# Optimization experiments

Hardware: AMD Instinct MI355X
Metric: run time of the kernel (lower is better)

The kernel has to match this reference:

```python
import jax, jax.numpy as jnp
import numpy as np

B, N = 16, 2048
EMB_DIM = 512
K = 20          # neighbor_num
S = 1           # support_num

def _norm(x, axis):
    # F.normalize: x / max(||x||, 1e-12)
    return x / jnp.maximum(jnp.linalg.norm(x, axis=axis, keepdims=True), 1e-12)

def knn(verts, k):
    # verts: (b, v, 3); squared-distance knn excluding self
    inner = jnp.einsum('bvd,bwd->bvw', verts, verts)
    quad = jnp.sum(verts * verts, axis=2)
    dist = quad[:, :, None] - 2.0 * inner + quad[:, None, :]
    _, idx = jax.lax.top_k(-dist, k + 1)
    return idx[:, :, 1:]

def gather_nb(x, idx):
    # x: (b, v, c), idx: (b, v, n) -> (b, v, n, c)
    return jax.vmap(lambda t, i: t[i])(x, idx)

def dir_norm(verts, idx):
    d = gather_nb(verts, idx) - verts[:, :, None, :]
    return _norm(d, -1)

def conv_surface(idx, verts, directions, kernel_num):
    theta = jax.nn.relu(jnp.einsum('bvnd,dk->bvnk', dir_norm(verts, idx), _norm(directions, 0)))
    b, v, n, _ = theta.shape
    theta = theta.reshape(b, v, n, S, kernel_num)
    return jnp.sum(jnp.max(theta, axis=2), axis=2)  # (b, v, kernel_num)

def conv_layer(idx, verts, fm, w, bias, directions, out_ch):
    theta = jax.nn.relu(jnp.einsum('bvnd,dk->bvnk', dir_norm(verts, idx), _norm(directions, 0)))
    feat = fm @ w + bias                            # (b, v, (S+1)*out_ch)
    center = feat[:, :, :out_ch]
    support = gather_nb(feat[:, :, out_ch:], idx)   # (b, v, n, S*out_ch)
    b, v, n, _ = support.shape
    act = (theta * support).reshape(b, v, n, S, out_ch)
    return center + jnp.sum(jnp.max(act, axis=2), axis=2)

def pool_layer(verts, fm, key, pooling_rate=4, neighbor_num=4):
    b, v, _ = verts.shape
    idx = knn(verts, neighbor_num)
    pooled = jnp.max(gather_nb(fm, idx), axis=2)
    samp = jax.random.permutation(key, v)[: v // pooling_rate]
    return verts[:, samp, :], pooled[:, samp, :]

def _forward(xyz, w1, b1, w2, b2, w3, b3, w4, b4, fcw, fcb, dir0,
             wc1, bc1, dir1, wc2, bc2, dir2, wc3, bc3, dir3, wc4, bc4, dir4,
             clw1, clb1, bn_gamma, bn_beta, clw2, clb2):
    relu = jax.nn.relu
    # PointNet trunk (Conv1d with kernel 1 == per-point matmul)
    x = relu(jnp.einsum('oc,bcn->bon', w1, xyz) + b1[None, :, None])
    x = relu(jnp.einsum('oc,bcn->bon', w2, x) + b2[None, :, None])
    gf = jnp.max(x, axis=2, keepdims=True)
    x = jnp.concatenate([x, jnp.broadcast_to(gf, x.shape)], axis=1)
    x = relu(jnp.einsum('oc,bcn->bon', w3, x) + b3[None, :, None])
    x = relu(jnp.einsum('oc,bcn->bon', w4, x) + b4[None, :, None])
    x = jnp.max(x, axis=2)                          # (B, 1024)
    # GCN3D trunk
    verts = jnp.transpose(xyz, (0, 2, 1))           # (B, N, 3)
    idx = knn(verts, K)
    fm0 = relu(conv_surface(idx, verts, dir0, 32))
    fm1 = relu(conv_layer(idx, verts, fm0, wc1, bc1, dir1, 64))
    verts, fm1 = pool_layer(verts, fm1, jax.random.key(1))
    idx = knn(verts, K)
    fm2 = relu(conv_layer(idx, verts, fm1, wc2, bc2, dir2, 128))
    fm3 = relu(conv_layer(idx, verts, fm2, wc3, bc3, dir3, 256))
    verts, fm3 = pool_layer(verts, fm3, jax.random.key(2))
    idx = knn(verts, K)
    fm4 = conv_layer(idx, verts, fm3, wc4, bc4, dir4, 1024)
    fg = jnp.max(fm4, axis=1)                       # (B, 1024)
    fc_data = jnp.concatenate([x, fg], axis=1)      # (B, 2048)
    embedding = fc_data @ fcw.T + fcb
    # classifier, eval mode: Dropout -> identity; BN uses running mean 0 / var 1
    h = fc_data @ clw1.T + clb1
    h = relu(h / jnp.sqrt(1.0 + 1e-5) * bn_gamma + bn_beta)
    pred = h @ clw2.T + clb2
    return embedding, pred

def setup_inputs():
    key = jax.random.key(0)
    ks = jax.random.split(key, 32)
    rn = lambda k, shp: jax.random.normal(k, shp, dtype=jnp.float32) * 0.05
    return {
        'xyz': jax.random.normal(ks[0], (B, 3, N), dtype=jnp.float32),
        'w1': rn(ks[1], (64, 3)), 'b1': rn(ks[2], (64,)),
        'w2': rn(ks[3], (128, 64)), 'b2': rn(ks[4], (128,)),
        'w3': rn(ks[5], (256, 256)), 'b3': rn(ks[6], (256,)),
        'w4': rn(ks[7], (1024, 256)), 'b4': rn(ks[8], (1024,)),
        'fcw': rn(ks[9], (EMB_DIM, 2048)), 'fcb': rn(ks[10], (EMB_DIM,)),
        'dir0': rn(ks[11], (3, 32)),
        'wc1': rn(ks[12], (32, 128)), 'bc1': rn(ks[13], (128,)), 'dir1': rn(ks[14], (3, 64)),
        'wc2': rn(ks[15], (64, 256)), 'bc2': rn(ks[16], (256,)), 'dir2': rn(ks[17], (3, 128)),
        'wc3': rn(ks[18], (128, 512)), 'bc3': rn(ks[19], (512,)), 'dir3': rn(ks[20], (3, 256)),
        'wc4': rn(ks[21], (256, 2048)), 'bc4': rn(ks[22], (2048,)), 'dir4': rn(ks[23], (3, 1024)),
        'clw1': rn(ks[24], (512, 2048)), 'clb1': rn(ks[25], (512,)),
        'bn_gamma': jnp.ones((512,), dtype=jnp.float32),
        'bn_beta': jnp.zeros((512,), dtype=jnp.float32),
        'clw2': rn(ks[26], (6, 512)), 'clb2': rn(ks[27], (6,)),
    }

def reference(xyz, w1, b1, w2, b2, w3, b3, w4, b4, fcw, fcb, dir0, wc1, bc1, dir1, wc2, bc2, dir2, wc3, bc3, dir3, wc4, bc4, dir4, clw1, clb1, bn_gamma, bn_beta, clw2, clb2):
    return _forward(xyz, w1, b1, w2, b2, w3, b3, w4, b4, fcw, fcb, dir0, wc1, bc1, dir1, wc2, bc2, dir2, wc3, bc3, dir3, wc4, bc4, dir4, clw1, clb1, bn_gamma, bn_beta, clw2, clb2)
```

## Files before the change

kernel.cpp:

```cpp
#include <hip/hip_runtime.h>
#include <hip/hip_bf16.h>
#include <math.h>

#define BB 16
#define NN 2048

typedef __attribute__((ext_vector_type(8))) short s8v;
typedef __attribute__((ext_vector_type(4))) float f4v;

__global__ void k_sentinel(float* o, int n, float v){
  int i = blockIdx.x*256 + threadIdx.x;
  if (i < n) o[i] = v;
}

__device__ __forceinline__ ushort f2bf(float x){
  unsigned u = __float_as_uint(x);
  unsigned r = u + 0x7FFFu + ((u>>16)&1u);
  return (ushort)(r>>16);
}
__device__ __forceinline__ void splitbf(float v, ushort &h, ushort &l){
  h = f2bf(v);
  float hf = __uint_as_float((unsigned)h<<16);
  l = f2bf(v-hf);
}


__global__ void k_wsrm(const float* __restrict__ src, ushort* __restrict__ dh,
                       ushort* __restrict__ dl, int total){
  int id = blockIdx.x*256 + threadIdx.x;
  if (id >= total) return;
  ushort h,l; splitbf(src[id], h, l);
  dh[id]=h; dl[id]=l;
}

__global__ void k_wstr(const float* __restrict__ src, ushort* __restrict__ dh,
                       ushort* __restrict__ dl, int K, int C){
  int id = blockIdx.x*256 + threadIdx.x;
  if (id >= K*C) return;
  int c = id % C, k = id / C;
  ushort h,l; splitbf(src[id], h, l);
  dh[(size_t)c*K + k]=h; dl[(size_t)c*K + k]=l;
}


__global__ void k_mlp1s(const float* __restrict__ xyz, const float* __restrict__ w1,
                        const float* __restrict__ b1, ushort* __restrict__ xh,
                        ushort* __restrict__ xl){
  int id = blockIdx.x*256 + threadIdx.x;
  if (id >= BB*NN*64) return;
  int o = id & 63, n = (id>>6) & (NN-1), b = id>>17;
  float acc = b1[o];
  #pragma unroll
  for (int c=0;c<3;c++)
    acc += w1[o*3+c] * xyz[(size_t)(b*3+c)*NN + n];
  acc = fmaxf(acc, 0.f);
  ushort h,l; splitbf(acc, h, l);
  xh[id]=h; xl[id]=l;
}

__global__ __launch_bounds__(256) void k_rowmax(const float* __restrict__ x, float* __restrict__ o,
                                                ushort* __restrict__ gh, ushort* __restrict__ gl, int cols){
  __shared__ float sm[256];
  int row = blockIdx.x, t = threadIdx.x;
  const float* xr = x + (size_t)row*cols;
  float m = -INFINITY;
  for (int c=t;c<cols;c+=256) m = fmaxf(m, xr[c]);
  sm[t]=m; __syncthreads();
  for (int s=128;s>0;s>>=1){ if (t<s) sm[t]=fmaxf(sm[t], sm[t+s]); __syncthreads(); }
  if (!t){
    o[row]=sm[0];
    ushort h,l; splitbf(sm[0], h, l);
    gh[row]=h; gl[row]=l;
  }
}

template<int EPI, int RELU, int BCOL>
__global__ __launch_bounds__(256) void k_bgemm(
    const ushort* __restrict__ Ahg, const ushort* __restrict__ Alg,
    const ushort* __restrict__ Bhg, const ushort* __restrict__ Blg,
    const ushort* __restrict__ gfh, const ushort* __restrict__ gfl,
    const float* __restrict__ bias,
    float* __restrict__ outp, float* __restrict__ pmaxp,
    ushort* __restrict__ oth, ushort* __restrict__ otl,
    int K, int ksplit, int Kb, int N, size_t sBT, size_t sOut, int M)
{
  __shared__ ushort Ah[128][40], Al[128][40];
  __shared__ ushort Bh[64][40],  Bl[64][40];
  __shared__ float red[2][128];
  int t = threadIdx.x, z = blockIdx.z;
  int o0 = blockIdx.y*128, n0 = blockIdx.x*64;
  int wid = t>>6, lane = t&63;
  int wm = wid>>1, wn = wid&1;
  int lr = lane&15, kg = lane>>4;

  f4v acc[4][2];
  #pragma unroll
  for (int i=0;i<4;i++)
    #pragma unroll
    for (int j=0;j<2;j++) acc[i][j] = (f4v){0.f,0.f,0.f,0.f};

  for (int k0=0; k0<K; k0+=32){
    __syncthreads();
    #pragma unroll
    for (int i=0;i<2;i++){
      int j = i*256+t, oo = j>>2, k8 = (j&3)*8;
      size_t sp = (size_t)(o0+oo)*K + k0 + k8;
      *(s8v*)&Ah[oo][k8] = *(const s8v*)(Ahg+sp);
      *(s8v*)&Al[oo][k8] = *(const s8v*)(Alg+sp);
    }
    {
      int nn = t>>2, k8 = (t&3)*8, gk = k0+k8;
      const ushort *sh, *sl;
      if (gk < ksplit){
        size_t sp = (size_t)z*sBT + (size_t)(n0+nn)*Kb + gk;
        sh = Bhg+sp; sl = Blg+sp;
      } else {
        size_t sp = (size_t)z*(K-ksplit) + (gk-ksplit);
        sh = gfh+sp; sl = gfl+sp;
      }
      *(s8v*)&Bh[nn][k8] = *(const s8v*)sh;
      *(s8v*)&Bl[nn][k8] = *(const s8v*)sl;
    }
    __syncthreads();

    s8v ah[4], al[4], bh[2], bl[2];
    #pragma unroll
    for (int mt=0;mt<4;mt++){
      int row = wm*64 + mt*16 + lr;
      ah[mt] = *(const s8v*)&Ah[row][kg*8];
      al[mt] = *(const s8v*)&Al[row][kg*8];
    }
    #pragma unroll
    for (int nt=0;nt<2;nt++){
      int col = wn*32 + nt*16 + lr;
      bh[nt] = *(const s8v*)&Bh[col][kg*8];
      bl[nt] = *(const s8v*)&Bl[col][kg*8];
    }
    #pragma unroll
    for (int mt=0;mt<4;mt++)
      #pragma unroll
      for (int nt=0;nt<2;nt++){
        acc[mt][nt] = __builtin_amdgcn_mfma_f32_16x16x32_bf16(ah[mt], bh[nt], acc[mt][nt], 0,0,0);
        acc[mt][nt] = __builtin_amdgcn_mfma_f32_16x16x32_bf16(ah[mt], bl[nt], acc[mt][nt], 0,0,0);
        acc[mt][nt] = __builtin_amdgcn_mfma_f32_16x16x32_bf16(al[mt], bh[nt], acc[mt][nt], 0,0,0);
      }
  }

  if (EPI == 1){
    #pragma unroll
    for (int mt=0;mt<4;mt++){
      #pragma unroll
      for (int e=0;e<4;e++){
        int row = o0 + wm*64 + mt*16 + kg*4 + e;
        float bv = bias[row];
        float m = fmaxf(fmaxf(acc[mt][0][e]+bv, 0.f), fmaxf(acc[mt][1][e]+bv, 0.f));
        m = fmaxf(m, __shfl_xor(m, 1, 64));
        m = fmaxf(m, __shfl_xor(m, 2, 64));
        m = fmaxf(m, __shfl_xor(m, 4, 64));
        m = fmaxf(m, __shfl_xor(m, 8, 64));
        if (lr == 0) red[wn][wm*64 + mt*16 + kg*4 + e] = m;
      }
    }
    __syncthreads();
    if (t < 128){
      float m = fmaxf(red[0][t], red[1][t]);
      pmaxp[((size_t)z*M + o0 + t)*gridDim.x + blockIdx.x] = m;
    }
  } else {
    #pragma unroll
    for (int mt=0;mt<4;mt++){
      #pragma unroll
      for (int nt=0;nt<2;nt++){
        int col = n0 + wn*32 + nt*16 + lr;
        #pragma unroll
        for (int e=0;e<4;e++){
          int row = o0 + wm*64 + mt*16 + kg*4 + e;
          float bv = BCOL ? bias[col] : bias[row];
          float v = acc[mt][nt][e] + bv;
          if (RELU) v = fmaxf(v, 0.f);
          if (EPI == 0 || EPI == 2)
            outp[(size_t)z*sOut + (size_t)row*N + col] = v;
          if (EPI >= 2){
            ushort h,l; splitbf(v, h, l);
            size_t p = ((size_t)z*N + col)*(size_t)M + row;
            oth[p]=h; otl[p]=l;
          }
        }
      }
    }
  }
}

__global__ void k_xmax(const float* __restrict__ pmax, float* __restrict__ xmax){
  int id = blockIdx.x*256 + threadIdx.x;
  if (id >= BB*1024) return;
  float m = pmax[(size_t)id*32];
  for (int k=1;k<32;k++) m = fmaxf(m, pmax[(size_t)id*32+k]);
  xmax[id] = m;
}


#define TF2BODY \
  unsigned ks2 = 0x1BD11BDAu ^ k0 ^ k1; \
  unsigned a = x0 + k0, b = x1 + k1; \
  { \
  a += b; b = (b<<13)|(b>>19); b ^= a; \
  a += b; b = (b<<15)|(b>>17); b ^= a; \
  a += b; b = (b<<26)|(b>>6);  b ^= a; \
  a += b; b = (b<<6) |(b>>26); b ^= a;  a += k1;  b += ks2 + 1u; \
  a += b; b = (b<<17)|(b>>15); b ^= a; \
  a += b; b = (b<<29)|(b>>3);  b ^= a; \
  a += b; b = (b<<16)|(b>>16); b ^= a; \
  a += b; b = (b<<24)|(b>>8);  b ^= a;  a += ks2; b += k0  + 2u; \
  a += b; b = (b<<13)|(b>>19); b ^= a; \
  a += b; b = (b<<15)|(b>>17); b ^= a; \
  a += b; b = (b<<26)|(b>>6);  b ^= a; \
  a += b; b = (b<<6) |(b>>26); b ^= a;  a += k0;  b += k1  + 3u; \
  a += b; b = (b<<17)|(b>>15); b ^= a; \
  a += b; b = (b<<29)|(b>>3);  b ^= a; \
  a += b; b = (b<<16)|(b>>16); b ^= a; \
  a += b; b = (b<<24)|(b>>8);  b ^= a;  a += k1;  b += ks2 + 4u; \
  a += b; b = (b<<13)|(b>>19); b ^= a; \
  a += b; b = (b<<15)|(b>>17); b ^= a; \
  a += b; b = (b<<26)|(b>>6);  b ^= a; \
  a += b; b = (b<<6) |(b>>26); b ^= a;  a += ks2; b += k0  + 5u; \
  } \
  o0 = a; o1 = b;

__device__ __forceinline__ void tf2(unsigned k0, unsigned k1, unsigned x0, unsigned x1,
                                    unsigned &o0, unsigned &o1){ TF2BODY }
static void tf2h(unsigned k0, unsigned k1, unsigned x0, unsigned x1,
                 unsigned &o0, unsigned &o1){ TF2BODY }

__global__ void k_permkeys(int n, unsigned sk0, unsigned sk1, unsigned* __restrict__ keys){
  int i = blockIdx.x*256 + threadIdx.x;
  if (i < n){ unsigned a,b2; tf2(sk0, sk1, 0u, (unsigned)i, a, b2); keys[i] = a ^ b2; }
}

__global__ void k_permrank(int n, const unsigned* __restrict__ keys,
                           const int* __restrict__ vin, int* __restrict__ vout){
  int i = blockIdx.x*256 + threadIdx.x;
  if (i >= n) return;
  unsigned ki = keys[i];
  int rank = 0;
  for (int j=0;j<n;j++){
    unsigned kj = keys[j];
    rank += (kj < ki) || (kj == ki && j < i);
  }
  vout[rank] = vin ? vin[i] : i;
}


__global__ void k_transpose(const float* __restrict__ xyz, float* __restrict__ verts){
  int id = blockIdx.x*256 + threadIdx.x;
  if (id >= BB*NN*3) return;
  int c = id % 3, v = (id/3) % NN, b = id/(3*NN);
  verts[id] = xyz[(size_t)(b*3+c)*NN + v];
}

template<int CPL, int KSEL>
__global__ __launch_bounds__(256,6) void k_knn_r(const float* __restrict__ vbcs,
                                                 const int* __restrict__ qmap, int numQ,
                                                 int* __restrict__ out){
  constexpr int V = CPL*64;
  constexpr int GS = (CPL < 8) ? CPL : 8;
  constexpr int NG = CPL/GS;
  constexpr int GSH = (GS==8)?3:((GS==4)?2:((GS==2)?1:0));
  int t = threadIdx.x, wid = t>>6, lane = t&63;
  int b = blockIdx.y;
  int q = blockIdx.x*4 + wid;
  if (q >= numQ) return;
  const float* vx = vbcs + (size_t)b*3*V;
  const float* vy = vx + V;
  const float* vz = vy + V;
  int qv = qmap ? qmap[q] : q;
  float qx = vx[qv], qy = vy[qv], qz = vz[qv];
  float qq = qx*qx + qy*qy + qz*qz;
  unsigned d[CPL];
  #pragma unroll
  for (int i=0;i<CPL;i++){
    int c = lane + i*64;
    float wx=vx[c], wy=vy[c], wz=vz[c];
    float inner = qx*wx + qy*wy + qz*wz;
    float ww = wx*wx + wy*wy + wz*wz;
    float dd = qq - 2.f*inner + ww;
    unsigned db = __float_as_uint(dd);
    d[i] = (db & 0x80000000u) ? ~db : (db | 0x80000000u);
  }
  unsigned long long g[NG];
  #pragma unroll
  for (int gg=0; gg<NG; gg++){
    unsigned long long m = ~0ull;
    #pragma unroll
    for (int j=0;j<GS;j++){
      int i = gg*GS+j;
      unsigned long long kk = ((unsigned long long)d[i]<<32) | (unsigned)(lane + i*64);
      m = (kk<m)?kk:m;
    }
    g[gg] = m;
  }
  unsigned long long lb = g[0];
  #pragma unroll
  for (int gg=1;gg<NG;gg++) lb = (g[gg]<lb)?g[gg]:lb;

  int* orow = out + ((size_t)b*numQ + q)*KSEL;
  unsigned long long last = 0ull;
  for (int r=0; r<=KSEL; r++){
    unsigned long long best = lb;
    #pragma unroll
    for (int off=32; off>0; off>>=1){
      unsigned long long o = __shfl_xor(best, off, 64);
      best = (o < best) ? o : best;
    }
    int c = (int)(best & 0xffffffffull);
    if (r>0 && lane==0) orow[r-1] = c;
    last = best;
    if ((c & 63) == lane){
      int gi = c >> (6 + GSH);
      #pragma unroll
      for (int gg=0; gg<NG; gg++){
        if (gg == gi){
          unsigned long long m = ~0ull;
          #pragma unroll
          for (int j=0;j<GS;j++){
            int i = gg*GS+j;
            unsigned long long kk = ((unsigned long long)d[i]<<32) | (unsigned)(lane + i*64);
            unsigned long long qk = (kk > last) ? kk : ~0ull;
            m = (qk<m)?qk:m;
          }
          g[gg] = m;
        }
      }
      unsigned long long nb2 = g[0];
      #pragma unroll
      for (int gg=1;gg<NG;gg++) nb2 = (g[gg]<nb2)?g[gg]:nb2;
      lb = nb2;
    }
  }
}

__global__ void k_poolidx(const int* __restrict__ idxsrc, const int* __restrict__ perm,
                          int* __restrict__ outp, int Vsrc, int numS, int total){
  int id = blockIdx.x*256 + threadIdx.x;
  if (id >= total) return;
  int j = id & 3, s = (id>>2) % numS, b = id/(numS*4);
  outp[id] = idxsrc[((size_t)b*Vsrc + perm[s])*20 + j];
}

__global__ void k_dirs(const float* __restrict__ verts, int V, const int* __restrict__ idx,
                       float* __restrict__ dirs, int total){
  int id = blockIdx.x*256 + threadIdx.x;
  if (id >= total) return;
  int v = (id/20) % V, b = id/(20*V);
  const float* vb = verts + (size_t)b*V*3;
  int nb = idx[id];
  float dx = vb[nb*3+0]-vb[v*3+0];
  float dy = vb[nb*3+1]-vb[v*3+1];
  float dz = vb[nb*3+2]-vb[v*3+2];
  float s = 1.f / fmaxf(sqrtf(dx*dx+dy*dy+dz*dz), 1e-12f);
  dirs[(size_t)id*3+0]=dx*s; dirs[(size_t)id*3+1]=dy*s; dirs[(size_t)id*3+2]=dz*s;
}

__global__ void k_surf(const float* __restrict__ dirs, const float* __restrict__ dir0,
                       ushort* __restrict__ fh, ushort* __restrict__ fl, int V){
  int id = blockIdx.x*256 + threadIdx.x;
  if (id >= BB*V*32) return;
  int k = id & 31; int vv = (id>>5) % V; int b = id/(32*V);
  float nx=dir0[k], ny=dir0[32+k], nz=dir0[64+k];
  float s = 1.f/fmaxf(sqrtf(nx*nx+ny*ny+nz*nz), 1e-12f);
  nx*=s; ny*=s; nz*=s;
  const float* dd = dirs + (size_t)(b*V+vv)*60;
  float m = 0.f;
  for (int n=0;n<20;n++){
    float th = dd[n*3]*nx + dd[n*3+1]*ny + dd[n*3+2]*nz;
    m = fmaxf(m, fmaxf(th, 0.f));
  }
  ushort h,l; splitbf(m, h, l);
  size_t p = (size_t)(b*V+vv)*32 + k;
  fh[p]=h; fl[p]=l;
}

template<int OUT>
__global__ void k_comb(const float* __restrict__ feat, const int* __restrict__ idx,
                       const float* __restrict__ dirs, const float* __restrict__ dw,
                       float* __restrict__ outp, ushort* __restrict__ oh, ushort* __restrict__ ol,
                       int V, int OC, int relu_flag){
  int id = blockIdx.x*256 + threadIdx.x;
  if (id >= BB*V*OC) return;
  int oc = id % OC, v = (id/OC) % V, b = id/(OC*V);
  float wx=dw[oc], wy=dw[OC+oc], wz=dw[2*OC+oc];
  float s = 1.f/fmaxf(sqrtf(wx*wx+wy*wy+wz*wz), 1e-12f);
  wx*=s; wy*=s; wz*=s;
  size_t row = (size_t)b*V + v;
  const int* ir = idx + row*20;
  const float* dd = dirs + row*60;
  float center = feat[row*2*OC + oc];
  float m = -INFINITY;
  for (int n=0;n<20;n++){
    int nb = ir[n];
    float th = dd[n*3]*wx + dd[n*3+1]*wy + dd[n*3+2]*wz;
    th = fmaxf(th, 0.f);
    float sup = feat[((size_t)b*V + nb)*2*OC + OC + oc];
    m = fmaxf(m, th*sup);
  }
  float rv = center + m;
  if (OUT == 0){
    outp[row*OC + oc] = relu_flag ? fmaxf(rv, 0.f) : rv;
  } else {
    rv = fmaxf(rv, 0.f);
    ushort h,l; splitbf(rv, h, l);
    oh[row*OC + oc]=h; ol[row*OC + oc]=l;
  }
}

template<int OUT>
__global__ void k_pool(const float* __restrict__ fm, const int* __restrict__ idx4,
                       float* __restrict__ outp, ushort* __restrict__ oh, ushort* __restrict__ ol,
                       int V, int C, int numS){
  int id = blockIdx.x*256 + threadIdx.x;
  if (id >= BB*numS*C) return;
  int c = id % C, sI = (id/C) % numS, b = id/(C*numS);
  const int* ir = idx4 + ((size_t)b*numS + sI)*4;
  float m = -INFINITY;
  for (int n=0;n<4;n++) m = fmaxf(m, fm[((size_t)b*V + ir[n])*C + c]);
  size_t p = ((size_t)b*numS + sI)*C + c;
  if (OUT == 0) outp[p] = m;
  else { ushort h,l; splitbf(m, h, l); oh[p]=h; ol[p]=l; }
}

__global__ void k_vgather(const float* __restrict__ vin, const int* __restrict__ perm,
                          float* __restrict__ vout, float* __restrict__ vbcs,
                          int V, int numS){
  int id = blockIdx.x*256 + threadIdx.x;
  if (id >= BB*numS*3) return;
  int c = id % 3, sI = (id/3) % numS, b = id/(3*numS);
  float val = vin[((size_t)b*V + perm[sI])*3 + c];
  vout[id] = val;
  vbcs[((size_t)b*3 + c)*numS + sI] = val;
}

__global__ void k_colmax(const float* __restrict__ x, float* __restrict__ o, int Vr, int C){
  int id = blockIdx.x*256 + threadIdx.x;
  if (id >= BB*C) return;
  int c = id % C, b = id / C;
  float m = -INFINITY;
  for (int v=0; v<Vr; v++) m = fmaxf(m, x[(size_t)(b*Vr+v)*C + c]);
  o[id] = m;
}


__global__ __launch_bounds__(256) void k_emb2(const float* __restrict__ xmax, const float* __restrict__ fg,
                                              const float* __restrict__ fcw, const float* __restrict__ fcb,
                                              float* __restrict__ outp){
  int gid = blockIdx.x*4 + (threadIdx.x>>6);
  int lane = threadIdx.x & 63;
  if (gid >= BB*512) return;
  int e = gid & 511, b = gid >> 9;
  const float* wr = fcw + (size_t)e*2048;
  const float* xb = xmax + b*1024;
  const float* gb = fg + b*1024;
  float acc = 0.f;
  for (int k=lane; k<1024; k+=64)
    acc += xb[k]*wr[k] + gb[k]*wr[1024+k];
  #pragma unroll
  for (int off=32; off>0; off>>=1) acc += __shfl_xor(acc, off, 64);
  if (lane==0) outp[gid] = acc + fcb[e];
}

__global__ __launch_bounds__(256) void k_h2(const float* __restrict__ xmax, const float* __restrict__ fg,
                                            const float* __restrict__ clw1, const float* __restrict__ clb1,
                                            const float* __restrict__ gamma, const float* __restrict__ beta,
                                            float* __restrict__ h){
  int gid = blockIdx.x*4 + (threadIdx.x>>6);
  int lane = threadIdx.x & 63;
  if (gid >= BB*512) return;
  int j = gid & 511, b = gid >> 9;
  const float* wr = clw1 + (size_t)j*2048;
  const float* xb = xmax + b*1024;
  const float* gb = fg + b*1024;
  float acc = 0.f;
  for (int k=lane; k<1024; k+=64)
    acc += xb[k]*wr[k] + gb[k]*wr[1024+k];
  #pragma unroll
  for (int off=32; off>0; off>>=1) acc += __shfl_xor(acc, off, 64);
  if (lane==0){
    const float inv_s = 1.0f / sqrtf(1.0f + 1e-5f);
    float v = (acc + clb1[j]) * inv_s * gamma[j] + beta[j];
    h[gid] = fmaxf(v, 0.f);
  }
}

__global__ __launch_bounds__(256) void k_pred2(const float* __restrict__ h, const float* __restrict__ clw2,
                                               const float* __restrict__ clb2, float* __restrict__ outp){
  int gid = blockIdx.x*4 + (threadIdx.x>>6);
  int lane = threadIdx.x & 63;
  if (gid >= BB*6) return;
  int o = gid % 6, b = gid / 6;
  const float* hb = h + b*512;
  const float* wr = clw2 + o*512;
  float acc = 0.f;
  for (int k=lane; k<512; k+=64) acc += hb[k]*wr[k];
  #pragma unroll
  for (int off=32; off>0; off>>=1) acc += __shfl_xor(acc, off, 64);
  if (lane==0) outp[BB*512 + gid] = acc + clb2[o];
}


static inline int cdiv(long long a, int b){ return (int)((a + b - 1)/b); }

extern "C" void kernel_launch(void* const* d_in, const int* in_sizes, int n_in,
                              void* d_out, int out_size, void* d_ws, size_t ws_size,
                              hipStream_t stream){
  float* out = (float*)d_out;
  if (n_in != 30 || in_sizes[0] != BB*3*NN || out_size != BB*512 + BB*6){
    k_sentinel<<<cdiv(out_size,256),256,0,stream>>>(out, out_size, 2000.0f);
    return;
  }
  const float* xyz  = (const float*)d_in[0];
  const float* w1   = (const float*)d_in[1];
  const float* b1   = (const float*)d_in[2];
  const float* w2   = (const float*)d_in[3];
  const float* b2   = (const float*)d_in[4];
  const float* w3   = (const float*)d_in[5];
  const float* b3   = (const float*)d_in[6];
  const float* w4   = (const float*)d_in[7];
  const float* b4   = (const float*)d_in[8];
  const float* fcw  = (const float*)d_in[9];
  const float* fcb  = (const float*)d_in[10];
  const float* dir0 = (const float*)d_in[11];
  const float* wc1  = (const float*)d_in[12];
  const float* bc1  = (const float*)d_in[13];
  const float* dir1 = (const float*)d_in[14];
  const float* wc2  = (const float*)d_in[15];
  const float* bc2  = (const float*)d_in[16];
  const float* dir2 = (const float*)d_in[17];
  const float* wc3  = (const float*)d_in[18];
  const float* bc3  = (const float*)d_in[19];
  const float* dir3 = (const float*)d_in[20];
  const float* wc4  = (const float*)d_in[21];
  const float* bc4  = (const float*)d_in[22];
  const float* dir4 = (const float*)d_in[23];
  const float* clw1 = (const float*)d_in[24];
  const float* clb1 = (const float*)d_in[25];
  const float* gma  = (const float*)d_in[26];
  const float* bta  = (const float*)d_in[27];
  const float* clw2 = (const float*)d_in[28];
  const float* clb2 = (const float*)d_in[29];

  char* w = (char*)d_ws;
  size_t off = 0;
  auto A = [&](size_t bytes){ size_t r = off; off += (bytes + 255) & ~(size_t)255; return r; };
  const size_t oXMAX = A((size_t)BB*1024*4);
  const size_t oFG   = A((size_t)BB*1024*4);
  const size_t oGF   = A((size_t)BB*128*4);
  const size_t oGFP  = A((size_t)BB*128*2*2);
  const size_t oH    = A((size_t)BB*512*4);
  const size_t oP2048= A(2048*4);
  const size_t oP512 = A(512*4);
  const size_t oPKEY = A(2048*4);
  const size_t oPA   = A(2048*4);
  const size_t oPMAX = A((size_t)BB*1024*32*4);
  const size_t oV0   = A((size_t)BB*2048*3*4);
  const size_t oV1   = A((size_t)BB*512*3*4);
  const size_t oV2   = A((size_t)BB*128*3*4);
  const size_t oV1S  = A((size_t)BB*3*512*4);
  const size_t oV2S  = A((size_t)BB*3*128*4);
  const size_t oIDX0 = A((size_t)BB*2048*20*4);
  const size_t oDIR0 = A((size_t)BB*2048*20*3*4);
  const size_t oFM0  = A((size_t)BB*2048*32*2*2);
  const size_t oFM1  = A((size_t)BB*2048*64*4);
  const size_t oI40  = A((size_t)BB*512*4*4);
  const size_t oFM1P = A((size_t)BB*512*64*2*2);
  const size_t oIDX1 = A((size_t)BB*512*20*4);
  const size_t oDIR1 = A((size_t)BB*512*20*3*4);
  const size_t oFM2  = A((size_t)BB*512*128*2*2);
  const size_t oFM3  = A((size_t)BB*512*256*4);
  const size_t oI41  = A((size_t)BB*128*4*4);
  const size_t oFM3P = A((size_t)BB*128*256*2*2);
  const size_t oIDX2 = A((size_t)BB*128*20*4);
  const size_t oDIR2 = A((size_t)BB*128*20*3*4);
  const size_t oFM4  = A((size_t)BB*128*1024*4);
  const size_t oBIGA = A((size_t)BB*256*NN*4);
  const size_t oBIGB = A((size_t)BB*128*NN*4);
  const size_t oW2P  = A((size_t)128*64*2*2);
  const size_t oW3P  = A((size_t)256*256*2*2);
  const size_t oW4P  = A((size_t)1024*256*2*2);
  const size_t oWC1T = A((size_t)32*128*2*2);
  const size_t oWC2T = A((size_t)64*256*2*2);
  const size_t oWC3T = A((size_t)128*512*2*2);
  const size_t oWC4T = A((size_t)256*2048*2*2);
  if (off > ws_size){
    k_sentinel<<<cdiv(out_size,256),256,0,stream>>>(out, out_size, 1000.0f);
    return;
  }
  float* xmax = (float*)(w+oXMAX); float* fg = (float*)(w+oFG);
  float* gf = (float*)(w+oGF);     float* hbuf = (float*)(w+oH);
  ushort* gfh = (ushort*)(w+oGFP); ushort* gfl = gfh + BB*128;
  int* p2048 = (int*)(w+oP2048);   int* p512 = (int*)(w+oP512);
  unsigned* pkeys = (unsigned*)(w+oPKEY); int* pa = (int*)(w+oPA);
  float* pmax = (float*)(w+oPMAX);
  float* v0 = (float*)(w+oV0); float* v1 = (float*)(w+oV1); float* v2 = (float*)(w+oV2);
  float* v1s = (float*)(w+oV1S); float* v2s = (float*)(w+oV2S);
  int* idx0 = (int*)(w+oIDX0); int* idx1 = (int*)(w+oIDX1); int* idx2 = (int*)(w+oIDX2);
  int* i40 = (int*)(w+oI40);   int* i41 = (int*)(w+oI41);
  float* d0 = (float*)(w+oDIR0); float* d1 = (float*)(w+oDIR1); float* d2 = (float*)(w+oDIR2);
  ushort* fm0h = (ushort*)(w+oFM0); ushort* fm0l = fm0h + (size_t)BB*2048*32;
  float* fm1 = (float*)(w+oFM1);
  ushort* fm1ph = (ushort*)(w+oFM1P); ushort* fm1pl = fm1ph + (size_t)BB*512*64;
  ushort* fm2h = (ushort*)(w+oFM2); ushort* fm2l = fm2h + (size_t)BB*512*128;
  float* fm3 = (float*)(w+oFM3);
  ushort* fm3ph = (ushort*)(w+oFM3P); ushort* fm3pl = fm3ph + (size_t)BB*128*256;
  float* fm4 = (float*)(w+oFM4);
  ushort* x1h = (ushort*)(w+oBIGA); ushort* x1l = x1h + (size_t)BB*2048*64;
  ushort* x3h = (ushort*)(w+oBIGA); ushort* x3l = x3h + (size_t)BB*2048*256;
  ushort* x2h = (ushort*)(w+oIDX0); ushort* x2l = x2h + (size_t)BB*2048*128;
  float* x2 = (float*)(w+oBIGB); float* feat = (float*)(w+oBIGB);
  ushort* w2ph = (ushort*)(w+oW2P); ushort* w2pl = w2ph + 128*64;
  ushort* w3ph = (ushort*)(w+oW3P); ushort* w3pl = w3ph + 256*256;
  ushort* w4ph = (ushort*)(w+oW4P); ushort* w4pl = w4ph + 1024*256;
  ushort* wc1h = (ushort*)(w+oWC1T); ushort* wc1l = wc1h + 32*128;
  ushort* wc2h = (ushort*)(w+oWC2T); ushort* wc2l = wc2h + 64*256;
  ushort* wc3h = (ushort*)(w+oWC3T); ushort* wc3l = wc3h + 128*512;
  ushort* wc4h = (ushort*)(w+oWC4T); ushort* wc4l = wc4h + 256*2048;

  k_wsrm<<<cdiv(128*64,256),256,0,stream>>>(w2, w2ph, w2pl, 128*64);
  k_wsrm<<<cdiv(256*256,256),256,0,stream>>>(w3, w3ph, w3pl, 256*256);
  k_wsrm<<<cdiv(1024*256,256),256,0,stream>>>(w4, w4ph, w4pl, 1024*256);
  k_wstr<<<cdiv(32*128,256),256,0,stream>>>(wc1, wc1h, wc1l, 32, 128);
  k_wstr<<<cdiv(64*256,256),256,0,stream>>>(wc2, wc2h, wc2l, 64, 256);
  k_wstr<<<cdiv(128*512,256),256,0,stream>>>(wc3, wc3h, wc3l, 128, 512);
  k_wstr<<<cdiv(256*2048,256),256,0,stream>>>(wc4, wc4h, wc4l, 256, 2048);

  k_mlp1s<<<cdiv((long long)BB*NN*64,256),256,0,stream>>>(xyz, w1, b1, x1h, x1l);
  k_bgemm<2,1,0><<<dim3(32,1,BB),256,0,stream>>>(w2ph, w2pl, x1h, x1l, nullptr, nullptr,
      b2, x2, nullptr, x2h, x2l, 64, 64, 64, 2048, (size_t)2048*64, (size_t)128*2048, 128);
  k_rowmax<<<BB*128,256,0,stream>>>(x2, gf, gfh, gfl, NN);
  k_bgemm<3,1,0><<<dim3(32,2,BB),256,0,stream>>>(w3ph, w3pl, x2h, x2l, gfh, gfl,
      b3, nullptr, nullptr, x3h, x3l, 256, 128, 128, 2048, (size_t)2048*128, 0, 256);
  k_bgemm<1,1,0><<<dim3(32,8,BB),256,0,stream>>>(w4ph, w4pl, x3h, x3l, nullptr, nullptr,
      b4, nullptr, pmax, nullptr, nullptr, 256, 256, 256, 2048, (size_t)2048*256, 0, 1024);
  k_xmax<<<cdiv(BB*1024,256),256,0,stream>>>(pmax, xmax);

  {
    unsigned ck0=0u, ck1=1u, nk0,nk1, s00,s01, s10,s11, sc0,sc1;
    tf2h(ck0,ck1, 0u,0u, nk0,nk1);
    tf2h(ck0,ck1, 0u,1u, s00,s01);
    tf2h(nk0,nk1, 0u,1u, s10,s11);
    tf2h(0u,2u,  0u,1u, sc0,sc1);
    k_permkeys<<<8,256,0,stream>>>(2048, s00, s01, pkeys);
    k_permrank<<<8,256,0,stream>>>(2048, pkeys, nullptr, pa);
    k_permkeys<<<8,256,0,stream>>>(2048, s10, s11, pkeys);
    k_permrank<<<8,256,0,stream>>>(2048, pkeys, pa, p2048);
    k_permkeys<<<2,256,0,stream>>>(512, sc0, sc1, pkeys);
    k_permrank<<<2,256,0,stream>>>(512, pkeys, nullptr, p512);
  }

  k_transpose<<<cdiv((long long)BB*NN*3,256),256,0,stream>>>(xyz, v0);
  k_knn_r<32,20><<<dim3(512,BB),256,0,stream>>>(xyz, nullptr, 2048, idx0);
  k_dirs<<<cdiv((long long)BB*2048*20,256),256,0,stream>>>(v0, 2048, idx0, d0, BB*2048*20);
  k_surf<<<cdiv((long long)BB*2048*32,256),256,0,stream>>>(d0, dir0, fm0h, fm0l, 2048);
  k_bgemm<0,0,1><<<dim3(2,256,1),256,0,stream>>>(fm0h, fm0l, wc1h, wc1l, nullptr, nullptr,
      bc1, feat, nullptr, nullptr, nullptr, 32, 32, 32, 128, 0, 0, BB*2048);
  k_comb<0><<<cdiv((long long)BB*2048*64,256),256,0,stream>>>(feat, idx0, d0, dir1, fm1, nullptr, nullptr, 2048, 64, 1);
  k_poolidx<<<cdiv(BB*512*4,256),256,0,stream>>>(idx0, p2048, i40, 2048, 512, BB*512*4);
  k_pool<1><<<cdiv((long long)BB*512*64,256),256,0,stream>>>(fm1, i40, nullptr, fm1ph, fm1pl, 2048, 64, 512);
  k_vgather<<<cdiv((long long)BB*512*3,256),256,0,stream>>>(v0, p2048, v1, v1s, 2048, 512);
  k_knn_r<8,20><<<dim3(128,BB),256,0,stream>>>(v1s, nullptr, 512, idx1);
  k_dirs<<<cdiv((long long)BB*512*20,256),256,0,stream>>>(v1, 512, idx1, d1, BB*512*20);
  k_bgemm<0,0,1><<<dim3(4,64,1),256,0,stream>>>(fm1ph, fm1pl, wc2h, wc2l, nullptr, nullptr,
      bc2, feat, nullptr, nullptr, nullptr, 64, 64, 64, 256, 0, 0, BB*512);
  k_comb<1><<<cdiv((long long)BB*512*128,256),256,0,stream>>>(feat, idx1, d1, dir2, nullptr, fm2h, fm2l, 512, 128, 1);
  k_bgemm<0,0,1><<<dim3(8,64,1),256,0,stream>>>(fm2h, fm2l, wc3h, wc3l, nullptr, nullptr,
      bc3, feat, nullptr, nullptr, nullptr, 128, 128, 128, 512, 0, 0, BB*512);
  k_comb<0><<<cdiv((long long)BB*512*256,256),256,0,stream>>>(feat, idx1, d1, dir3, fm3, nullptr, nullptr, 512, 256, 1);
  k_poolidx<<<cdiv(BB*128*4,256),256,0,stream>>>(idx1, p512, i41, 512, 128, BB*128*4);
  k_pool<1><<<cdiv((long long)BB*128*256,256),256,0,stream>>>(fm3, i41, nullptr, fm3ph, fm3pl, 512, 256, 128);
  k_vgather<<<cdiv((long long)BB*128*3,256),256,0,stream>>>(v1, p512, v2, v2s, 512, 128);
  k_knn_r<2,20><<<dim3(32,BB),256,0,stream>>>(v2s, nullptr, 128, idx2);
  k_dirs<<<cdiv((long long)BB*128*20,256),256,0,stream>>>(v2, 128, idx2, d2, BB*128*20);
  k_bgemm<0,0,1><<<dim3(32,16,1),256,0,stream>>>(fm3ph, fm3pl, wc4h, wc4l, nullptr, nullptr,
      bc4, feat, nullptr, nullptr, nullptr, 256, 256, 256, 2048, 0, 0, BB*128);
  k_comb<0><<<cdiv((long long)BB*128*1024,256),256,0,stream>>>(feat, idx2, d2, dir4, fm4, nullptr, nullptr, 128, 1024, 0);
  k_colmax<<<cdiv(BB*1024,256),256,0,stream>>>(fm4, fg, 128, 1024);

  k_emb2<<<cdiv(BB*512,4),256,0,stream>>>(xmax, fg, fcw, fcb, out);
  k_h2<<<cdiv(BB*512,4),256,0,stream>>>(xmax, fg, clw1, clb1, gma, bta, hbuf);
  k_pred2<<<cdiv(BB*6,4),256,0,stream>>>(hbuf, clw2, clb2, out);
}
```

Baseline: 764.0 us.

## Batch weight-split and perm-key launches, fuse rowmax into GEMM, shuffle-32 knn

Several prep launches are merged. The seven weight-split kernels become two, and the three permutation-key kernels become one. The conv2 GEMM now writes per-tile partial maxima and bf16 outputs directly, so the fp32 x2 store and separate rowmax pass go away, replaced by a small partial-max reduce. The knn top-k selection now reduces 32-bit distances across the wavefront with a ballot to pick the winning lane instead of 64-bit shuffles, and the launch bound drops to 4 waves per SIMD. The knn tie-breaking order changes to lane-first, and occupancy may differ.

```diff
diff --git a/kernel.cpp b/kernel.cpp
--- a/kernel.cpp
+++ b/kernel.cpp
@@ -25,20 +25,33 @@
 }
 
 
-__global__ void k_wsrm(const float* __restrict__ src, ushort* __restrict__ dh,
-                       ushort* __restrict__ dl, int total){
-  int id = blockIdx.x*256 + threadIdx.x;
-  if (id >= total) return;
-  ushort h,l; splitbf(src[id], h, l);
-  dh[id]=h; dl[id]=l;
-}
-
-__global__ void k_wstr(const float* __restrict__ src, ushort* __restrict__ dh,
-                       ushort* __restrict__ dl, int K, int C){
-  int id = blockIdx.x*256 + threadIdx.x;
-  if (id >= K*C) return;
-  int c = id % C, k = id / C;
-  ushort h,l; splitbf(src[id], h, l);
+__global__ void k_wsplit3(const float* __restrict__ s1, ushort* __restrict__ d1h, ushort* __restrict__ d1l, int n1,
+                          const float* __restrict__ s2, ushort* __restrict__ d2h, ushort* __restrict__ d2l, int n2,
+                          const float* __restrict__ s3, ushort* __restrict__ d3h, ushort* __restrict__ d3l, int n3){
+  int id = blockIdx.x*256 + threadIdx.x;
+  const float* s; ushort *dh, *dl; int i;
+  if (id < n1){ s=s1; dh=d1h; dl=d1l; i=id; }
+  else if (id < n1+n2){ s=s2; dh=d2h; dl=d2l; i=id-n1; }
+  else if (id < n1+n2+n3){ s=s3; dh=d3h; dl=d3l; i=id-n1-n2; }
+  else return;
+  ushort h,l; splitbf(s[i], h, l);
+  dh[i]=h; dl[i]=l;
+}
+
+__global__ void k_wstr4(const float* __restrict__ s1, ushort* __restrict__ d1h, ushort* __restrict__ d1l, int K1, int C1,
+                        const float* __restrict__ s2, ushort* __restrict__ d2h, ushort* __restrict__ d2l, int K2, int C2,
+                        const float* __restrict__ s3, ushort* __restrict__ d3h, ushort* __restrict__ d3l, int K3, int C3,
+                        const float* __restrict__ s4, ushort* __restrict__ d4h, ushort* __restrict__ d4l, int K4, int C4){
+  int id = blockIdx.x*256 + threadIdx.x;
+  int n1=K1*C1, n2=K2*C2, n3=K3*C3, n4=K4*C4;
+  const float* s; ushort *dh, *dl; int i, K, C;
+  if (id < n1){ s=s1; dh=d1h; dl=d1l; i=id; K=K1; C=C1; }
+  else if (id < n1+n2){ s=s2; dh=d2h; dl=d2l; i=id-n1; K=K2; C=C2; }
+  else if (id < n1+n2+n3){ s=s3; dh=d3h; dl=d3l; i=id-n1-n2; K=K3; C=C3; }
+  else if (id < n1+n2+n3+n4){ s=s4; dh=d4h; dl=d4l; i=id-n1-n2-n3; K=K4; C=C4; }
+  else return;
+  int c = i % C, k = i / C;
+  ushort h,l; splitbf(s[i], h, l);
   dh[(size_t)c*K + k]=h; dl[(size_t)c*K + k]=l;
 }
 
@@ -58,20 +71,14 @@
   xh[id]=h; xl[id]=l;
 }
 
-__global__ __launch_bounds__(256) void k_rowmax(const float* __restrict__ x, float* __restrict__ o,
-                                                ushort* __restrict__ gh, ushort* __restrict__ gl, int cols){
-  __shared__ float sm[256];
-  int row = blockIdx.x, t = threadIdx.x;
-  const float* xr = x + (size_t)row*cols;
-  float m = -INFINITY;
-  for (int c=t;c<cols;c+=256) m = fmaxf(m, xr[c]);
-  sm[t]=m; __syncthreads();
-  for (int s=128;s>0;s>>=1){ if (t<s) sm[t]=fmaxf(sm[t], sm[t+s]); __syncthreads(); }
-  if (!t){
-    o[row]=sm[0];
-    ushort h,l; splitbf(sm[0], h, l);
-    gh[row]=h; gl[row]=l;
-  }
+__global__ void k_gmax(const float* __restrict__ pmax, ushort* __restrict__ gh,
+                       ushort* __restrict__ gl, int parts, int total){
+  int id = blockIdx.x*256 + threadIdx.x;
+  if (id >= total) return;
+  float m = pmax[(size_t)id*parts];
+  for (int k=1;k<parts;k++) m = fmaxf(m, pmax[(size_t)id*parts+k]);
+  ushort h,l; splitbf(m, h, l);
+  gh[id]=h; gl[id]=l;
 }
 
 template<int EPI, int RELU, int BCOL>
@@ -146,14 +153,26 @@
       }
   }
 
-  if (EPI == 1){
+  if (EPI == 1 || EPI == 4){
     #pragma unroll
     for (int mt=0;mt<4;mt++){
       #pragma unroll
       for (int e=0;e<4;e++){
         int row = o0 + wm*64 + mt*16 + kg*4 + e;
         float bv = bias[row];
-        float m = fmaxf(fmaxf(acc[mt][0][e]+bv, 0.f), fmaxf(acc[mt][1][e]+bv, 0.f));
+        float v0 = fmaxf(acc[mt][0][e]+bv, 0.f);
+        float v1 = fmaxf(acc[mt][1][e]+bv, 0.f);
+        if (EPI == 4){
+          int col0 = n0 + wn*32 + lr;
+          ushort h,l;
+          splitbf(v0, h, l);
+          size_t p0 = ((size_t)z*N + col0)*(size_t)M + row;
+          oth[p0]=h; otl[p0]=l;
+          splitbf(v1, h, l);
+          size_t p1 = ((size_t)z*N + col0+16)*(size_t)M + row;
+          oth[p1]=h; otl[p1]=l;
+        }
+        float m = fmaxf(v0, v1);
         m = fmaxf(m, __shfl_xor(m, 1, 64));
         m = fmaxf(m, __shfl_xor(m, 2, 64));
         m = fmaxf(m, __shfl_xor(m, 4, 64));
@@ -178,9 +197,9 @@
           float bv = BCOL ? bias[col] : bias[row];
           float v = acc[mt][nt][e] + bv;
           if (RELU) v = fmaxf(v, 0.f);
-          if (EPI == 0 || EPI == 2)
+          if (EPI == 0)
             outp[(size_t)z*sOut + (size_t)row*N + col] = v;
-          if (EPI >= 2){
+          if (EPI == 3){
             ushort h,l; splitbf(v, h, l);
             size_t p = ((size_t)z*N + col)*(size_t)M + row;
             oth[p]=h; otl[p]=l;
@@ -232,9 +251,13 @@
 static void tf2h(unsigned k0, unsigned k1, unsigned x0, unsigned x1,
                  unsigned &o0, unsigned &o1){ TF2BODY }
 
-__global__ void k_permkeys(int n, unsigned sk0, unsigned sk1, unsigned* __restrict__ keys){
-  int i = blockIdx.x*256 + threadIdx.x;
-  if (i < n){ unsigned a,b2; tf2(sk0, sk1, 0u, (unsigned)i, a, b2); keys[i] = a ^ b2; }
+__global__ void k_permkeys3(unsigned a0, unsigned a1, unsigned* __restrict__ ka,
+                            unsigned b0, unsigned b1, unsigned* __restrict__ kb,
+                            unsigned c0, unsigned c1, unsigned* __restrict__ kc){
+  int id = blockIdx.x*256 + threadIdx.x;
+  if (id < 2048){ unsigned x,y; tf2(a0,a1, 0u,(unsigned)id, x,y); ka[id] = x^y; }
+  if (id < 2048){ unsigned x,y; tf2(b0,b1, 0u,(unsigned)id, x,y); kb[id] = x^y; }
+  if (id < 512){ unsigned x,y; tf2(c0,c1, 0u,(unsigned)id, x,y); kc[id] = x^y; }
 }
 
 __global__ void k_permrank(int n, const unsigned* __restrict__ keys,
@@ -259,13 +282,11 @@
 }
 
 template<int CPL, int KSEL>
-__global__ __launch_bounds__(256,6) void k_knn_r(const float* __restrict__ vbcs,
-                                                 const int* __restrict__ qmap, int numQ,
-                                                 int* __restrict__ out){
+__global__ __launch_bounds__(256,4) void k_knn_s(const float* __restrict__ vbcs,
+                                                 int numQ, int* __restrict__ out){
   constexpr int V = CPL*64;
   constexpr int GS = (CPL < 8) ? CPL : 8;
   constexpr int NG = CPL/GS;
-  constexpr int GSH = (GS==8)?3:((GS==4)?2:((GS==2)?1:0));
   int t = threadIdx.x, wid = t>>6, lane = t&63;
   int b = blockIdx.y;
   int q = blockIdx.x*4 + wid;
@@ -273,8 +294,7 @@
   const float* vx = vbcs + (size_t)b*3*V;
   const float* vy = vx + V;
   const float* vz = vy + V;
-  int qv = qmap ? qmap[q] : q;
-  float qx = vx[qv], qy = vy[qv], qz = vz[qv];
+  float qx = vx[q], qy = vy[q], qz = vz[q];
   float qq = qx*qx + qy*qy + qz*qz;
   unsigned d[CPL];
   #pragma unroll
@@ -293,48 +313,51 @@
     unsigned long long m = ~0ull;
     #pragma unroll
     for (int j=0;j<GS;j++){
-      int i = gg*GS+j;
-      unsigned long long kk = ((unsigned long long)d[i]<<32) | (unsigned)(lane + i*64);
+      int p = gg*GS+j;
+      unsigned long long kk = ((unsigned long long)d[p]<<32) | (unsigned)p;
       m = (kk<m)?kk:m;
     }
     g[gg] = m;
   }
-  unsigned long long lb = g[0];
+  unsigned lmin = (unsigned)(g[0]>>32);
   #pragma unroll
-  for (int gg=1;gg<NG;gg++) lb = (g[gg]<lb)?g[gg]:lb;
+  for (int gg=1;gg<NG;gg++){ unsigned x = (unsigned)(g[gg]>>32); lmin = (x<lmin)?x:lmin; }
 
   int* orow = out + ((size_t)b*numQ + q)*KSEL;
-  unsigned long long last = 0ull;
   for (int r=0; r<=KSEL; r++){
-    unsigned long long best = lb;
+    unsigned bd = lmin;
     #pragma unroll
     for (int off=32; off>0; off>>=1){
-      unsigned long long o = __shfl_xor(best, off, 64);
-      best = (o < best) ? o : best;
-    }
-    int c = (int)(best & 0xffffffffull);
-    if (r>0 && lane==0) orow[r-1] = c;
-    last = best;
-    if ((c & 63) == lane){
-      int gi = c >> (6 + GSH);
+      unsigned o = __shfl_xor(bd, off, 64);
+      bd = (o < bd) ? o : bd;
+    }
+    unsigned long long bal = __ballot(lmin == bd);
+    int winner = __ffsll(bal) - 1;
+    if (lane == winner){
+      unsigned long long mbest = g[0];
+      #pragma unroll
+      for (int gg=1;gg<NG;gg++) mbest = (g[gg]<mbest)?g[gg]:mbest;
+      int pos = (int)(mbest & 0xffffffffull);
+      if (r>0) orow[r-1] = lane + pos*64;
+      int gi = pos / GS;
       #pragma unroll
       for (int gg=0; gg<NG; gg++){
         if (gg == gi){
           unsigned long long m = ~0ull;
           #pragma unroll
           for (int j=0;j<GS;j++){
-            int i = gg*GS+j;
-            unsigned long long kk = ((unsigned long long)d[i]<<32) | (unsigned)(lane + i*64);
-            unsigned long long qk = (kk > last) ? kk : ~0ull;
-            m = (qk<m)?qk:m;
+            int p = gg*GS+j;
+            unsigned long long kk = ((unsigned long long)d[p]<<32) | (unsigned)p;
+            if (kk <= mbest) kk = ~0ull;
+            m = (kk<m)?kk:m;
           }
           g[gg] = m;
         }
       }
-      unsigned long long nb2 = g[0];
+      unsigned nl = (unsigned)(g[0]>>32);
       #pragma unroll
-      for (int gg=1;gg<NG;gg++) nb2 = (g[gg]<nb2)?g[gg]:nb2;
-      lb = nb2;
+      for (int gg=1;gg<NG;gg++){ unsigned x = (unsigned)(g[gg]>>32); nl = (x<nl)?x:nl; }
+      lmin = nl;
     }
   }
 }
@@ -552,12 +575,13 @@
   auto A = [&](size_t bytes){ size_t r = off; off += (bytes + 255) & ~(size_t)255; return r; };
   const size_t oXMAX = A((size_t)BB*1024*4);
   const size_t oFG   = A((size_t)BB*1024*4);
-  const size_t oGF   = A((size_t)BB*128*4);
   const size_t oGFP  = A((size_t)BB*128*2*2);
   const size_t oH    = A((size_t)BB*512*4);
   const size_t oP2048= A(2048*4);
   const size_t oP512 = A(512*4);
-  const size_t oPKEY = A(2048*4);
+  const size_t oPK1  = A(2048*4);
+  const size_t oPK2  = A(2048*4);
+  const size_t oPK3  = A(512*4);
   const size_t oPA   = A(2048*4);
   const size_t oPMAX = A((size_t)BB*1024*32*4);
   const size_t oV0   = A((size_t)BB*2048*3*4);
@@ -594,10 +618,11 @@
     return;
   }
   float* xmax = (float*)(w+oXMAX); float* fg = (float*)(w+oFG);
-  float* gf = (float*)(w+oGF);     float* hbuf = (float*)(w+oH);
+  float* hbuf = (float*)(w+oH);
   ushort* gfh = (ushort*)(w+oGFP); ushort* gfl = gfh + BB*128;
   int* p2048 = (int*)(w+oP2048);   int* p512 = (int*)(w+oP512);
-  unsigned* pkeys = (unsigned*)(w+oPKEY); int* pa = (int*)(w+oPA);
+  unsigned* pk1 = (unsigned*)(w+oPK1); unsigned* pk2 = (unsigned*)(w+oPK2);
+  unsigned* pk3 = (unsigned*)(w+oPK3); int* pa = (int*)(w+oPA);
   float* pmax = (float*)(w+oPMAX);
   float* v0 = (float*)(w+oV0); float* v1 = (float*)(w+oV1); float* v2 = (float*)(w+oV2);
   float* v1s = (float*)(w+oV1S); float* v2s = (float*)(w+oV2S);
@@ -614,7 +639,7 @@
   ushort* x1h = (ushort*)(w+oBIGA); ushort* x1l = x1h + (size_t)BB*2048*64;
   ushort* x3h = (ushort*)(w+oBIGA); ushort* x3l = x3h + (size_t)BB*2048*256;
   ushort* x2h = (ushort*)(w+oIDX0); ushort* x2l = x2h + (size_t)BB*2048*128;
-  float* x2 = (float*)(w+oBIGB); float* feat = (float*)(w+oBIGB);
+  float* feat = (float*)(w+oBIGB);
   ushort* w2ph = (ushort*)(w+oW2P); ushort* w2pl = w2ph + 128*64;
   ushort* w3ph = (ushort*)(w+oW3P); ushort* w3pl = w3ph + 256*256;
   ushort* w4ph = (ushort*)(w+oW4P); ushort* w4pl = w4ph + 1024*256;
@@ -623,18 +648,16 @@
   ushort* wc3h = (ushort*)(w+oWC3T); ushort* wc3l = wc3h + 128*512;
   ushort* wc4h = (ushort*)(w+oWC4T); ushort* wc4l = wc4h + 256*2048;
 
-  k_wsrm<<<cdiv(128*64,256),256,0,stream>>>(w2, w2ph, w2pl, 128*64);
-  k_wsrm<<<cdiv(256*256,256),256,0,stream>>>(w3, w3ph, w3pl, 256*256);
-  k_wsrm<<<cdiv(1024*256,256),256,0,stream>>>(w4, w4ph, w4pl, 1024*256);
-  k_wstr<<<cdiv(32*128,256),256,0,stream>>>(wc1, wc1h, wc1l, 32, 128);
-  k_wstr<<<cdiv(64*256,256),256,0,stream>>>(wc2, wc2h, wc2l, 64, 256);
-  k_wstr<<<cdiv(128*512,256),256,0,stream>>>(wc3, wc3h, wc3l, 128, 512);
-  k_wstr<<<cdiv(256*2048,256),256,0,stream>>>(wc4, wc4h, wc4l, 256, 2048);
+  k_wsplit3<<<cdiv(128*64+256*256+1024*256,256),256,0,stream>>>(
+      w2, w2ph, w2pl, 128*64,  w3, w3ph, w3pl, 256*256,  w4, w4ph, w4pl, 1024*256);
+  k_wstr4<<<cdiv(32*128+64*256+128*512+256*2048,256),256,0,stream>>>(
+      wc1, wc1h, wc1l, 32, 128,  wc2, wc2h, wc2l, 64, 256,
+      wc3, wc3h, wc3l, 128, 512, wc4, wc4h, wc4l, 256, 2048);
 
   k_mlp1s<<<cdiv((long long)BB*NN*64,256),256,0,stream>>>(xyz, w1, b1, x1h, x1l);
-  k_bgemm<2,1,0><<<dim3(32,1,BB),256,0,stream>>>(w2ph, w2pl, x1h, x1l, nullptr, nullptr,
-      b2, x2, nullptr, x2h, x2l, 64, 64, 64, 2048, (size_t)2048*64, (size_t)128*2048, 128);
-  k_rowmax<<<BB*128,256,0,stream>>>(x2, gf, gfh, gfl, NN);
+  k_bgemm<4,1,0><<<dim3(32,1,BB),256,0,stream>>>(w2ph, w2pl, x1h, x1l, nullptr, nullptr,
+      b2, nullptr, pmax, x2h, x2l, 64, 64, 64, 2048, (size_t)2048*64, 0, 128);
+  k_gmax<<<cdiv(BB*128,256),256,0,stream>>>(pmax, gfh, gfl, 32, BB*128);
   k_bgemm<3,1,0><<<dim3(32,2,BB),256,0,stream>>>(w3ph, w3pl, x2h, x2l, gfh, gfl,
       b3, nullptr, nullptr, x3h, x3l, 256, 128, 128, 2048, (size_t)2048*128, 0, 256);
   k_bgemm<1,1,0><<<dim3(32,8,BB),256,0,stream>>>(w4ph, w4pl, x3h, x3l, nullptr, nullptr,
@@ -647,16 +670,14 @@
     tf2h(ck0,ck1, 0u,1u, s00,s01);
     tf2h(nk0,nk1, 0u,1u, s10,s11);
     tf2h(0u,2u,  0u,1u, sc0,sc1);
-    k_permkeys<<<8,256,0,stream>>>(2048, s00, s01, pkeys);
-    k_permrank<<<8,256,0,stream>>>(2048, pkeys, nullptr, pa);
-    k_permkeys<<<8,256,0,stream>>>(2048, s10, s11, pkeys);
-    k_permrank<<<8,256,0,stream>>>(2048, pkeys, pa, p2048);
-    k_permkeys<<<2,256,0,stream>>>(512, sc0, sc1, pkeys);
-    k_permrank<<<2,256,0,stream>>>(512, pkeys, nullptr, p512);
+    k_permkeys3<<<8,256,0,stream>>>(s00,s01,pk1, s10,s11,pk2, sc0,sc1,pk3);
+    k_permrank<<<8,256,0,stream>>>(2048, pk1, nullptr, pa);
+    k_permrank<<<8,256,0,stream>>>(2048, pk2, pa, p2048);
+    k_permrank<<<2,256,0,stream>>>(512, pk3, nullptr, p512);
   }
 
   k_transpose<<<cdiv((long long)BB*NN*3,256),256,0,stream>>>(xyz, v0);
-  k_knn_r<32,20><<<dim3(512,BB),256,0,stream>>>(xyz, nullptr, 2048, idx0);
+  k_knn_s<32,20><<<dim3(512,BB),256,0,stream>>>(xyz, 2048, idx0);
   k_dirs<<<cdiv((long long)BB*2048*20,256),256,0,stream>>>(v0, 2048, idx0, d0, BB*2048*20);
   k_surf<<<cdiv((long long)BB*2048*32,256),256,0,stream>>>(d0, dir0, fm0h, fm0l, 2048);
   k_bgemm<0,0,1><<<dim3(2,256,1),256,0,stream>>>(fm0h, fm0l, wc1h, wc1l, nullptr, nullptr,
@@ -665,7 +686,7 @@
   k_poolidx<<<cdiv(BB*512*4,256),256,0,stream>>>(idx0, p2048, i40, 2048, 512, BB*512*4);
   k_pool<1><<<cdiv((long long)BB*512*64,256),256,0,stream>>>(fm1, i40, nullptr, fm1ph, fm1pl, 2048, 64, 512);
   k_vgather<<<cdiv((long long)BB*512*3,256),256,0,stream>>>(v0, p2048, v1, v1s, 2048, 512);
-  k_knn_r<8,20><<<dim3(128,BB),256,0,stream>>>(v1s, nullptr, 512, idx1);
+  k_knn_s<8,20><<<dim3(128,BB),256,0,stream>>>(v1s, 512, idx1);
   k_dirs<<<cdiv((long long)BB*512*20,256),256,0,stream>>>(v1, 512, idx1, d1, BB*512*20);
   k_bgemm<0,0,1><<<dim3(4,64,1),256,0,stream>>>(fm1ph, fm1pl, wc2h, wc2l, nullptr, nullptr,
       bc2, feat, nullptr, nullptr, nullptr, 64, 64, 64, 256, 0, 0, BB*512);
@@ -676,7 +697,7 @@
   k_poolidx<<<cdiv(BB*128*4,256),256,0,stream>>>(idx1, p512, i41, 512, 128, BB*128*4);
   k_pool<1><<<cdiv((long long)BB*128*256,256),256,0,stream>>>(fm3, i41, nullptr, fm3ph, fm3pl, 512, 256, 128);
   k_vgather<<<cdiv((long long)BB*128*3,256),256,0,stream>>>(v1, p512, v2, v2s, 512, 128);
-  k_knn_r<2,20><<<dim3(32,BB),256,0,stream>>>(v2s, nullptr, 128, idx2);
+  k_knn_s<2,20><<<dim3(32,BB),256,0,stream>>>(v2s, 128, idx2);
   k_dirs<<<cdiv((long long)BB*128*20,256),256,0,stream>>>(v2, 128, idx2, d2, BB*128*20);
   k_bgemm<0,0,1><<<dim3(32,16,1),256,0,stream>>>(fm3ph, fm3pl, wc4h, wc4l, nullptr, nullptr,
       bc4, feat, nullptr, nullptr, nullptr, 256, 256, 256, 2048, 0, 0, BB*128);
```

After: 718.1 us. 1.06x faster.
